# Performance work log

Measured on AMD Instinct MI355X. Metric: run time of the kernel, lower is better.

The kernel has to match this reference:

```python
import jax, jax.numpy as jnp
import numpy as np
from jax import lax

B, CIN, H, W = 4, 64, 256, 256
Q, K = 256, 16


def _conv3x3_replicate(x, w, b):
    # replicate (edge) padding of 1, then VALID conv -> same spatial size
    xp = jnp.pad(x, ((0, 0), (0, 0), (1, 1), (1, 1)), mode='edge')
    y = lax.conv_general_dilated(xp, w, (1, 1), 'VALID',
                                 dimension_numbers=('NCHW', 'OIHW', 'NCHW'))
    return y + b[None, :, None, None]


def setup_inputs() -> dict:
    key = jax.random.key(0)
    ks = jax.random.split(key, 9)
    s1 = 1.0 / np.sqrt(CIN * 9)
    s2 = 1.0 / np.sqrt(Q * 9)
    s3 = 1.0 / np.sqrt(Q)
    return {
        'x':  jax.random.normal(ks[0], (B, CIN, H, W), jnp.float32),
        'w1': jax.random.normal(ks[1], (Q, CIN, 3, 3), jnp.float32) * s1,
        'b1': jax.random.normal(ks[2], (Q,), jnp.float32) * s1,
        'w2': jax.random.normal(ks[3], (Q, Q, 3, 3), jnp.float32) * s2,
        'b2': jax.random.normal(ks[4], (Q,), jnp.float32) * s2,
        'w3': jax.random.normal(ks[5], (Q, Q, 1, 1), jnp.float32) * s3,
        'b3': jax.random.normal(ks[6], (Q,), jnp.float32) * s3,
        'mu': jax.random.normal(ks[7], (K, Q), jnp.float32),      # cluster_mu squeezed
        'label': jax.random.normal(ks[8], (K,), jnp.float32),
    }


def reference(x, w1, b1, w2, b2, w3, b3, mu, label):
    # query_encoder: Convx2 (conv3x3 replicate + relu, twice) then 1x1 conv
    q = jax.nn.relu(_conv3x3_replicate(x, w1, b1))
    q = jax.nn.relu(_conv3x3_replicate(q, w2, b2))
    q = jnp.einsum('oc,bchw->bohw', w3[:, :, 0, 0], q) + b3[None, :, None, None]
    # logit[b,k,h,w] = -sum_c (q - mu)^2, via norm expansion (no BxKxCxHxW tensor)
    q2 = jnp.sum(q * q, axis=1, keepdims=True)                   # (B,1,H,W)
    mu2 = jnp.sum(mu * mu, axis=1)                               # (K,)
    cross = jnp.einsum('bchw,kc->bkhw', q, mu)                   # (B,K,H,W)
    logit = -(q2 - 2.0 * cross + mu2[None, :, None, None])
    att = jax.nn.softmax(logit, axis=1)                          # softmax over clusters
    out = jnp.einsum('bkhw,k->bhw', att, label)
    return out[:, None]                                          # (B,1,H,W)
```

## Files before the change

### kernel.cpp

```cpp
#include <hip/hip_runtime.h>

#define BB   4
#define CIN  64
#define HH   256
#define WW   256
#define QQ   256
#define KK   16

typedef _Float16 half8 __attribute__((ext_vector_type(8)));
typedef float   f32x16 __attribute__((ext_vector_type(16)));
typedef unsigned int u32;

#define OFF_W1R   0ull
#define OFF_W2R   294912ull
#define OFF_WMU   1474560ull
#define OFF_LGB   1490944ull
#define OFF_ACT0  1605888ull
#define OFF_ACT1  35160320ull

__device__ __forceinline__ void dma16(const void* g, void* l) {
  __builtin_amdgcn_global_load_lds(
      (const __attribute__((address_space(1))) u32*)g,
      (__attribute__((address_space(3))) u32*)l, 16, 0, 0);
}

__global__ __launch_bounds__(256) void k_prep(
    const float* __restrict__ w1, const float* __restrict__ w2,
    const float* __restrict__ w3, const float* __restrict__ b3,
    const float* __restrict__ mu,
    _Float16* __restrict__ w1r, _Float16* __restrict__ w2r,
    float* __restrict__ wpart, float* __restrict__ lgb) {
  int bid = blockIdx.x, tid = threadIdx.x;
  if (bid < 576) {
    int idx = bid * 256 + tid;
    int blk = idx >> 13;
    int cc = blk / 9, tt = blk - cc * 9;
    int rem = idx & 8191;
    int n = rem >> 5, r = rem & 31;
    int q = (r >> 3) ^ ((n >> 1) & 3), e = r & 7;
    int c = cc * 32 + q * 8 + e;
    w1r[idx] = (_Float16)w1[(n * 64 + c) * 9 + tt];
  } else if (bid < 2880) {
    int d = (bid - 576) * 256 + tid;
    int blk = d >> 13;
    int cc = blk / 9, tt = blk - cc * 9;
    int rem = d & 8191;
    int n = rem >> 5, r = rem & 31;
    int q = (r >> 3) ^ ((n >> 1) & 3), e = r & 7;
    int c = cc * 32 + q * 8 + e;
    w2r[d] = (_Float16)w2[(n * 256 + c) * 9 + tt];
  } else if (bid < 3008) {
    int j = bid - 2880;
    int k = j >> 3, o0 = (j & 7) << 5;
    float s = 0.f;
#pragma unroll 4
    for (int oi = 0; oi < 32; ++oi) {
      int o = o0 + oi;
      s = fmaf(mu[k * 256 + o], w3[o * 256 + tid], s);
    }
    wpart[j * 256 + tid] = s;
  } else {
    int k = bid - 3008;
    float m = mu[k * 256 + tid];
    __shared__ float red[256];
    red[tid] = m * (2.f * b3[tid] - m);
    __syncthreads();
    for (int st = 128; st > 0; st >>= 1) {
      if (tid < st) red[tid] += red[tid + st];
      __syncthreads();
    }
    if (tid == 0) lgb[k] = red[0];
  }
}

__global__ __launch_bounds__(256) void k_prep2(
    const float* __restrict__ wpart, float* __restrict__ wmu2) {
  int k = blockIdx.x, tid = threadIdx.x;
  float s = 0.f;
#pragma unroll
  for (int p = 0; p < 8; ++p) s += wpart[(k * 8 + p) * 256 + tid];
  wmu2[k * 256 + tid] = 2.f * s;
}

__global__ __launch_bounds__(256) void k_t0(const float* __restrict__ x,
                                            _Float16* __restrict__ act0) {
  __shared__ float tile[64][65];
  int blk = blockIdx.x;
  int b = blk >> 10;
  int p0 = (blk & 1023) << 6;
  int t = threadIdx.x;
  {
    int p = t & 63, c0 = t >> 6;
    const float* xb = x + (size_t)b * (CIN * 65536) + p0 + p;
#pragma unroll
    for (int i = 0; i < 16; ++i) {
      int c = c0 + (i << 2);
      tile[c][p] = xb[(size_t)c * 65536];
    }
  }
  __syncthreads();
  {
    _Float16* o = act0 + (size_t)(b * 65536 + p0) * CIN;
#pragma unroll
    for (int uu = 0; uu < 2; ++uu) {
      int u = t + (uu << 8);
      int px = u & 63, oct = u >> 6;
      half8 h;
#pragma unroll
      for (int i = 0; i < 8; ++i) h[i] = (_Float16)tile[oct * 8 + i][px];
      *(half8*)(o + px * CIN + oct * 8) = h;
    }
  }
}

template <int CI>
__global__ __launch_bounds__(256, 2) void k_conv(
    const _Float16* __restrict__ actin, const char* __restrict__ wr,
    const float* __restrict__ bias, _Float16* __restrict__ actout) {
  constexpr int NC = CI / 32;
  constexpr int NT = 9 * NC;
  __shared__ __align__(16) char smem[73728];
  auto As = (char(*)[12288])smem;
  auto Bs = (char(*)[16384])(smem + 24576);
  _Float16* Qs = (_Float16*)smem;

  int tid = threadIdx.x;
  int b = blockIdx.x >> 9;
  int tile = blockIdx.x & 511;
  int txi = tile & 15, tyi = tile >> 4;
  int x0 = txi << 4, y0 = tyi << 3;
  int lane = tid & 63, wave = tid >> 6;
  int mwave = wave >> 1, nwave = wave & 1;
  int l31 = lane & 31, khalf = lane >> 5;

  f32x16 acc[2][4];
#pragma unroll
  for (int s = 0; s < 2; ++s)
#pragma unroll
    for (int nt = 0; nt < 4; ++nt)
#pragma unroll
      for (int r = 0; r < 16; ++r) acc[s][nt][r] = 0.f;

  const char* aG[3];
  int aL[3];
#pragma unroll
  for (int i = 0; i < 3; ++i) {
    int px = (wave * 3 + i) * 16 + (lane >> 2);
    int s = lane & 3;
    int pxc = min(px, 179);
    int hy = pxc / 18, hx = pxc - hy * 18;
    int y = min(max(y0 - 1 + hy, 0), 255);
    int x = min(max(x0 - 1 + hx, 0), 255);
    int q = s ^ ((pxc >> 1) & 3);
    aG[i] = (const char*)actin +
            (((size_t)(b * 65536 + y * 256 + x)) * CI + q * 8) * 2;
    aL[i] = (wave * 3 + i) * 1024;
  }
  const char* bG = wr + wave * 4096 + lane * 16;
  int bL = wave * 4096;

#pragma unroll
  for (int i = 0; i < 3; ++i) dma16(aG[i], &As[0][aL[i]]);
#pragma unroll
  for (int i = 0; i < 4; ++i) dma16(bG + i * 1024, &Bs[0][bL + i * 1024]);
#pragma unroll
  for (int i = 0; i < 4; ++i)
    dma16(bG + 16384 + i * 1024, &Bs[1][bL + i * 1024]);
  asm volatile("s_waitcnt vmcnt(4)" ::: "memory");
  __builtin_amdgcn_s_barrier();

  for (int cc = 0; cc < NC; ++cc) {
#pragma unroll
    for (int t = 0; t < 9; ++t) {
      int j = cc * 9 + t;
      if (t == 8 && cc + 1 < NC) {
#pragma unroll
        for (int i = 0; i < 3; ++i)
          dma16(aG[i] + (cc + 1) * 64, &As[(cc + 1) & 1][aL[i]]);
      }
      bool pf = (j + 2 < NT);
      if (pf) {
        const char* bsrc = bG + (size_t)(j + 2) * 16384;
        char* bdst = &Bs[(t + 2) % 3][bL];
#pragma unroll
        for (int i = 0; i < 4; ++i) dma16(bsrc + i * 1024, bdst + i * 1024);
      }
      int dy = t / 3, dx = t - dy * 3;
      const char* Ab = As[cc & 1];
      const char* Bb = Bs[t % 3];
      half8 af[2][2], bf[2][4];
#pragma unroll
      for (int s = 0; s < 2; ++s) {
        int px = (mwave * 4 + s * 2 + (l31 >> 4) + dy) * 18 + (l31 & 15) + dx;
        int sw = ((px >> 1) & 3) << 4;
#pragma unroll
        for (int ks = 0; ks < 2; ++ks) {
          int q = (ks * 2 + khalf) << 4;
          af[ks][s] = *(const half8*)(Ab + px * 64 + (q ^ sw));
        }
      }
#pragma unroll
      for (int nt = 0; nt < 4; ++nt) {
        int n = nwave * 128 + nt * 32 + l31;
        int sw = ((n >> 1) & 3) << 4;
#pragma unroll
        for (int ks = 0; ks < 2; ++ks) {
          int q = (ks * 2 + khalf) << 4;
          bf[ks][nt] = *(const half8*)(Bb + n * 64 + (q ^ sw));
        }
      }
      __builtin_amdgcn_s_setprio(1);
#pragma unroll
      for (int ks = 0; ks < 2; ++ks)
#pragma unroll
        for (int s = 0; s < 2; ++s)
#pragma unroll
          for (int nt = 0; nt < 4; ++nt)
            acc[s][nt] = __builtin_amdgcn_mfma_f32_32x32x16_f16(
                af[ks][s], bf[ks][nt], acc[s][nt], 0, 0, 0);
      __builtin_amdgcn_s_setprio(0);
      if (pf)
        asm volatile("s_waitcnt vmcnt(4) lgkmcnt(0)" ::: "memory");
      else
        asm volatile("s_waitcnt vmcnt(0) lgkmcnt(0)" ::: "memory");
      __builtin_amdgcn_s_barrier();
    }
  }

#pragma unroll
  for (int s = 0; s < 2; ++s)
#pragma unroll
    for (int nt = 0; nt < 4; ++nt) {
      int n = nwave * 128 + nt * 32 + l31;
      float bn = bias[n];
#pragma unroll
      for (int r = 0; r < 16; ++r) {
        int mrow = (r & 3) + 8 * (r >> 2) + 4 * khalf;
        int p = (mwave * 4 + s * 2 + (mrow >> 4)) * 16 + (mrow & 15);
        Qs[p * 264 + n] = (_Float16)fmaxf(acc[s][nt][r] + bn, 0.f);
      }
    }
  __syncthreads();
  {
    _Float16* gout = actout + (((size_t)(b * 65536 + y0 * 256 + x0)) << 8);
#pragma unroll
    for (int i = 0; i < 16; ++i) {
      int f = tid + (i << 8);
      int p = f >> 5, o = f & 31;
      half8 v = *(const half8*)&Qs[p * 264 + o * 8];
      *(half8*)(gout + (((p >> 4) * 256 + (p & 15)) << 8) + o * 8) = v;
    }
  }
}

__global__ __launch_bounds__(256) void k_head(
    const _Float16* __restrict__ a2_0, const _Float16* __restrict__ a2_1,
    const _Float16* __restrict__ a2_2, const _Float16* __restrict__ a2_3,
    const float* __restrict__ wmu2, const float* __restrict__ lgb,
    const float* __restrict__ label, float* __restrict__ out) {
  int b = blockIdx.x >> 8;
  int px = (blockIdx.x & 255) * 256 + threadIdx.x;
  const _Float16* base = (b == 0) ? a2_0 : (b == 1) ? a2_1
                       : (b == 2) ? a2_2 : a2_3;
  const half8* ap = (const half8*)(base + ((size_t)px << 8));
  float cr[16];
#pragma unroll
  for (int k = 0; k < 16; ++k) cr[k] = lgb[k];
#pragma unroll 2
  for (int cc = 0; cc < 32; ++cc) {
    half8 h = ap[cc];
    float a0 = (float)h[0], a1 = (float)h[1], a2 = (float)h[2],
          a3 = (float)h[3], a4 = (float)h[4], a5 = (float)h[5],
          a6 = (float)h[6], a7 = (float)h[7];
#pragma unroll
    for (int k = 0; k < 16; ++k) {
      const float* w = wmu2 + (k << 8) + (cc << 3);
      float c0 = cr[k];
      c0 = fmaf(a0, w[0], c0);
      c0 = fmaf(a1, w[1], c0);
      c0 = fmaf(a2, w[2], c0);
      c0 = fmaf(a3, w[3], c0);
      c0 = fmaf(a4, w[4], c0);
      c0 = fmaf(a5, w[5], c0);
      c0 = fmaf(a6, w[6], c0);
      c0 = fmaf(a7, w[7], c0);
      cr[k] = c0;
    }
  }
  float mx = cr[0];
#pragma unroll
  for (int k = 1; k < 16; ++k) mx = fmaxf(mx, cr[k]);
  float num = 0.f, den = 0.f;
#pragma unroll
  for (int k = 0; k < 16; ++k) {
    float e = __expf(cr[k] - mx);
    num = fmaf(e, label[k], num);
    den += e;
  }
  out[(size_t)b * 65536 + px] = num / den;
}

extern "C" void kernel_launch(void* const* d_in, const int* in_sizes, int n_in,
                              void* d_out, int out_size, void* d_ws, size_t ws_size,
                              hipStream_t stream) {
  const float* x  = (const float*)d_in[0];
  const float* w1 = (const float*)d_in[1];
  const float* b1 = (const float*)d_in[2];
  const float* w2 = (const float*)d_in[3];
  const float* b2 = (const float*)d_in[4];
  const float* w3 = (const float*)d_in[5];
  const float* b3 = (const float*)d_in[6];
  const float* mu = (const float*)d_in[7];
  const float* label = (const float*)d_in[8];
  float* out = (float*)d_out;

  char* ws = (char*)d_ws;
  _Float16* w1r  = (_Float16*)(ws + OFF_W1R);
  _Float16* w2r  = (_Float16*)(ws + OFF_W2R);
  float*    wmu2 = (float*)   (ws + OFF_WMU);
  float*    lgb  = (float*)   (ws + OFF_LGB);
  _Float16* act0 = (_Float16*)(ws + OFF_ACT0);
  _Float16* act1 = (_Float16*)(ws + OFF_ACT1);
  float*    wpart = (float*)  (ws + OFF_ACT1);

  _Float16* a2d[4] = {
    (_Float16*)(ws + OFF_ACT0),
    act1 + 0 * (size_t)65536 * 256,
    act1 + 1 * (size_t)65536 * 256,
    act1 + 2 * (size_t)65536 * 256
  };

  k_prep<<<3024, 256, 0, stream>>>(w1, w2, w3, b3, mu, w1r, w2r, wpart, lgb);
  k_prep2<<<16, 256, 0, stream>>>(wpart, wmu2);
  k_t0<<<4096, 256, 0, stream>>>(x, act0);
  k_conv<64><<<2048, 256, 0, stream>>>(act0, (const char*)w1r, b1, act1);
  for (int b = 0; b < BB; ++b)
    k_conv<256><<<512, 256, 0, stream>>>(act1 + (size_t)b * 65536 * 256,
                                         (const char*)w2r, b2, a2d[b]);
  k_head<<<1024, 256, 0, stream>>>(a2d[0], a2d[1], a2d[2], a2d[3],
                                   wmu2, lgb, label, out);
}
```

Before: 588.0 us.

## Software-pipeline conv LDS fragment loads across k-halves and deepen weight prefetch

Restructures the conv main loop so each tap splits into two k-halves. The second half's fragments are loaded from LDS while the MFMAs for the first half run, and the next tap's first-half fragments are loaded after the barrier, overlapping LDS reads with matrix math. Weight prefetch now goes three stages ahead instead of two, and activation prefetch moves earlier, which needs retuned vmcnt waits. This adds register pressure from double-buffered fragments and makes the waitcnt logic more fragile.

```diff
diff --git a/kernel.cpp b/kernel.cpp
--- a/kernel.cpp
+++ b/kernel.cpp
@@ -121,7 +121,6 @@
   constexpr int NT = 9 * NC;
   __shared__ __align__(16) char smem[73728];
   auto As = (char(*)[12288])smem;
-  auto Bs = (char(*)[16384])(smem + 24576);
   _Float16* Qs = (_Float16*)smem;
 
   int tid = threadIdx.x;
@@ -159,71 +158,111 @@
   const char* bG = wr + wave * 4096 + lane * 16;
   int bL = wave * 4096;
 
+  int bo[4];
+#pragma unroll
+  for (int nt = 0; nt < 4; ++nt) {
+    int n = nwave * 128 + nt * 32 + l31;
+    bo[nt] = n * 64 + ((khalf << 4) ^ (((n >> 1) & 3) << 4));
+  }
+  int pxA = (mwave * 4 + (l31 >> 4)) * 18 + (l31 & 15);
+
 #pragma unroll
   for (int i = 0; i < 3; ++i) dma16(aG[i], &As[0][aL[i]]);
 #pragma unroll
-  for (int i = 0; i < 4; ++i) dma16(bG + i * 1024, &Bs[0][bL + i * 1024]);
-#pragma unroll
-  for (int i = 0; i < 4; ++i)
-    dma16(bG + 16384 + i * 1024, &Bs[1][bL + i * 1024]);
+  for (int bufi = 0; bufi < 3; ++bufi)
+#pragma unroll
+    for (int i = 0; i < 4; ++i)
+      dma16(bG + bufi * 16384 + i * 1024,
+            smem + 24576 + bufi * 16384 + bL + i * 1024);
   asm volatile("s_waitcnt vmcnt(4)" ::: "memory");
   __builtin_amdgcn_s_barrier();
 
+  half8 af0[2], af1[2], bf0[4], bf1[4];
+  {
+    const char* Ab = As[0];
+    const char* Bb = smem + 24576;
+#pragma unroll
+    for (int s = 0; s < 2; ++s) {
+      int px = pxA + s * 36;
+      int a = px * 64 + ((khalf << 4) ^ (((px >> 1) & 3) << 4));
+      af0[s] = *(const half8*)(Ab + a);
+    }
+#pragma unroll
+    for (int nt = 0; nt < 4; ++nt) bf0[nt] = *(const half8*)(Bb + bo[nt]);
+  }
+
   for (int cc = 0; cc < NC; ++cc) {
+    const char* Ab = As[cc & 1];
+    const char* Abn = As[(cc + 1) & 1];
 #pragma unroll
     for (int t = 0; t < 9; ++t) {
       int j = cc * 9 + t;
-      if (t == 8 && cc + 1 < NC) {
+      const char* Bb = smem + 24576 + (t % 3) * 16384;
+      const char* Bbn = smem + 24576 + ((t + 1) % 3) * 16384;
+      int D = (t / 3) * 18 + (t % 3);
+#pragma unroll
+      for (int s = 0; s < 2; ++s) {
+        int px = pxA + s * 36 + D;
+        int a = px * 64 + ((((2 + khalf)) << 4) ^ (((px >> 1) & 3) << 4));
+        af1[s] = *(const half8*)(Ab + a);
+      }
+#pragma unroll
+      for (int nt = 0; nt < 4; ++nt)
+        bf1[nt] = *(const half8*)(Bb + (bo[nt] ^ 32));
+      __builtin_amdgcn_s_setprio(1);
+#pragma unroll
+      for (int s = 0; s < 2; ++s)
+#pragma unroll
+        for (int nt = 0; nt < 4; ++nt)
+          acc[s][nt] = __builtin_amdgcn_mfma_f32_32x32x16_f16(
+              af0[s], bf0[nt], acc[s][nt], 0, 0, 0);
+      __builtin_amdgcn_s_setprio(0);
+      if (t <= 6) {
+        asm volatile("s_waitcnt vmcnt(4) lgkmcnt(0)" ::: "memory");
+      } else if (t == 7) {
+        if (cc + 1 < NC)
+          asm volatile("s_waitcnt vmcnt(7) lgkmcnt(0)" ::: "memory");
+        else
+          asm volatile("s_waitcnt vmcnt(0) lgkmcnt(0)" ::: "memory");
+      } else {
+        if (cc + 1 < NC)
+          asm volatile("s_waitcnt vmcnt(4) lgkmcnt(0)" ::: "memory");
+        else
+          asm volatile("s_waitcnt vmcnt(0) lgkmcnt(0)" ::: "memory");
+      }
+      __builtin_amdgcn_s_barrier();
+      if (t == 6 && cc + 1 < NC) {
 #pragma unroll
         for (int i = 0; i < 3; ++i)
           dma16(aG[i] + (cc + 1) * 64, &As[(cc + 1) & 1][aL[i]]);
       }
-      bool pf = (j + 2 < NT);
-      if (pf) {
-        const char* bsrc = bG + (size_t)(j + 2) * 16384;
-        char* bdst = &Bs[(t + 2) % 3][bL];
+      if (j + 3 < NT) {
+        const char* bsrc = bG + (size_t)(j + 3) * 16384;
+        char* bdst = smem + 24576 + (t % 3) * 16384 + bL;
 #pragma unroll
         for (int i = 0; i < 4; ++i) dma16(bsrc + i * 1024, bdst + i * 1024);
       }
-      int dy = t / 3, dx = t - dy * 3;
-      const char* Ab = As[cc & 1];
-      const char* Bb = Bs[t % 3];
-      half8 af[2][2], bf[2][4];
-#pragma unroll
-      for (int s = 0; s < 2; ++s) {
-        int px = (mwave * 4 + s * 2 + (l31 >> 4) + dy) * 18 + (l31 & 15) + dx;
-        int sw = ((px >> 1) & 3) << 4;
-#pragma unroll
-        for (int ks = 0; ks < 2; ++ks) {
-          int q = (ks * 2 + khalf) << 4;
-          af[ks][s] = *(const half8*)(Ab + px * 64 + (q ^ sw));
+      if (j + 1 < NT) {
+        const char* An = (t < 8) ? Ab : Abn;
+        int Dn = (t < 8) ? (((t + 1) / 3) * 18 + ((t + 1) % 3)) : 0;
+#pragma unroll
+        for (int s = 0; s < 2; ++s) {
+          int px = pxA + s * 36 + Dn;
+          int a = px * 64 + ((khalf << 4) ^ (((px >> 1) & 3) << 4));
+          af0[s] = *(const half8*)(An + a);
         }
-      }
-#pragma unroll
-      for (int nt = 0; nt < 4; ++nt) {
-        int n = nwave * 128 + nt * 32 + l31;
-        int sw = ((n >> 1) & 3) << 4;
-#pragma unroll
-        for (int ks = 0; ks < 2; ++ks) {
-          int q = (ks * 2 + khalf) << 4;
-          bf[ks][nt] = *(const half8*)(Bb + n * 64 + (q ^ sw));
-        }
+#pragma unroll
+        for (int nt = 0; nt < 4; ++nt)
+          bf0[nt] = *(const half8*)(Bbn + bo[nt]);
       }
       __builtin_amdgcn_s_setprio(1);
 #pragma unroll
-      for (int ks = 0; ks < 2; ++ks)
-#pragma unroll
-        for (int s = 0; s < 2; ++s)
-#pragma unroll
-          for (int nt = 0; nt < 4; ++nt)
-            acc[s][nt] = __builtin_amdgcn_mfma_f32_32x32x16_f16(
-                af[ks][s], bf[ks][nt], acc[s][nt], 0, 0, 0);
+      for (int s = 0; s < 2; ++s)
+#pragma unroll
+        for (int nt = 0; nt < 4; ++nt)
+          acc[s][nt] = __builtin_amdgcn_mfma_f32_32x32x16_f16(
+              af1[s], bf1[nt], acc[s][nt], 0, 0, 0);
       __builtin_amdgcn_s_setprio(0);
-      if (pf)
-        asm volatile("s_waitcnt vmcnt(4) lgkmcnt(0)" ::: "memory");
-      else
-        asm volatile("s_waitcnt vmcnt(0) lgkmcnt(0)" ::: "memory");
-      __builtin_amdgcn_s_barrier();
     }
   }
 
```

After: 597.9 us. About the same (+1.7%).
